# Kernel tuning notes

Measured on AMD Instinct MI355X. Metric: run time of the kernel, lower is better.

The kernel has to match this reference:

```python
import jax, jax.numpy as jnp
import numpy as np
import math

B, T, C = 2, 2048, 1024
N_HEAD = 16
HEAD_DIM = C // N_HEAD


def setup_inputs() -> dict:
    key = jax.random.key(0)
    k1, k2, k3 = jax.random.split(key, 3)
    x = jax.random.normal(k1, (B, T, C), dtype=jnp.float32)
    # causal mask: positions where mask == 0 get -inf
    mask = jnp.tril(jnp.ones((T, T), dtype=bool))[None, None, :, :]
    W_attn = jax.random.normal(k2, (C, 3 * C), dtype=jnp.float32) * (1.0 / math.sqrt(C))
    b_attn = jnp.zeros((3 * C,), dtype=jnp.float32)
    W_proj = jax.random.normal(k3, (C, C), dtype=jnp.float32) * (1.0 / math.sqrt(C))
    b_proj = jnp.zeros((C,), dtype=jnp.float32)
    return {"x": x, "mask": mask, "W_attn": W_attn, "b_attn": b_attn,
            "W_proj": W_proj, "b_proj": b_proj}


def reference(x, mask, W_attn, b_attn, W_proj, b_proj):
    Bx, Tx, Cx = x.shape
    qkv = x @ W_attn + b_attn                      # [B,T,3C]
    q, k, v = jnp.split(qkv, 3, axis=2)
    # [B,T,C] -> [B,H,T,D]
    q = q.reshape(Bx, Tx, N_HEAD, HEAD_DIM).transpose(0, 2, 1, 3)
    k = k.reshape(Bx, Tx, N_HEAD, HEAD_DIM).transpose(0, 2, 1, 3)
    v = v.reshape(Bx, Tx, N_HEAD, HEAD_DIM).transpose(0, 2, 1, 3)
    scale = 1.0 / math.sqrt(HEAD_DIM)
    att = jnp.einsum('bhqd,bhkd->bhqk', q, k) * scale   # [B,H,T,T]
    att = jnp.where(mask, att, -jnp.inf)
    att = jax.nn.softmax(att, axis=-1)
    y = jnp.einsum('bhqk,bhkd->bhqd', att, v)            # [B,H,T,D]
    y = y.transpose(0, 2, 1, 3).reshape(Bx, Tx, Cx)      # [B,T,C]
    return y @ W_proj + b_proj
```

## Files before the change

### kernel.cpp

```cpp
#include <hip/hip_runtime.h>
#include <hip/hip_bf16.h>
#include <cstdint>

typedef unsigned short u16;
typedef unsigned int u32;
typedef unsigned long long u64;
using f32x4 = __attribute__((ext_vector_type(4))) float;
using s16x8 = __attribute__((ext_vector_type(8))) short;
using u32x4 = __attribute__((ext_vector_type(4))) u32;

#define NB 2
#define NT 2048
#define NC 1024
#define NH 16
#define HD 64

__device__ __forceinline__ u16 f2b(float f) {
    unsigned u = __float_as_uint(f);
    unsigned r = (u + 0x7FFFu + ((u >> 16) & 1u)) >> 16;
    return (u16)r;
}

__device__ __forceinline__ u32 cvtpk(float a, float b) {
    u32 r;
    asm("v_cvt_pk_bf16_f32 %0, %1, %2" : "=v"(r) : "v"(a), "v"(b));
    return r;
}
__device__ __forceinline__ void swap32(u32& a, u32& b) {
    asm("v_permlane32_swap_b32 %0, %1" : "+v"(a), "+v"(b));
}
__device__ __forceinline__ void swap16(u32& a, u32& b) {
    asm("v_permlane16_swap_b32 %0, %1" : "+v"(a), "+v"(b));
}

__device__ __forceinline__ void gl_lds16(const void* g, const void* l) {
    __builtin_amdgcn_global_load_lds(
        (const __attribute__((address_space(1))) unsigned int*)g,
        (__attribute__((address_space(3))) unsigned int*)l, 16, 0, 0);
}

__global__ __launch_bounds__(256) void conv_bf16(const float* __restrict__ in,
                                                 u16* __restrict__ out, int n4) {
    int i = blockIdx.x * 256 + threadIdx.x;
    if (i >= n4) return;
    float4 v = ((const float4*)in)[i];
    u64 pack = (u64)f2b(v.x) | ((u64)f2b(v.y) << 16) |
               ((u64)f2b(v.z) << 32) | ((u64)f2b(v.w) << 48);
    ((u64*)out)[i] = pack;
}

__global__ __launch_bounds__(256) void transpose_bf16(const float* __restrict__ W,
                                                      u16* __restrict__ Wt,
                                                      int K, int N) {
    __shared__ u16 s[64][65];
    const int n0 = blockIdx.x * 64, k0 = blockIdx.y * 64;
    const int t = threadIdx.x;
    const int tr = t >> 4, tc4 = (t & 15) * 4;
#pragma unroll
    for (int i = 0; i < 4; i++) {
        int r = tr + i * 16;
        float4 v = *(const float4*)&W[(size_t)(k0 + r) * N + n0 + tc4];
        s[r][tc4 + 0] = f2b(v.x);
        s[r][tc4 + 1] = f2b(v.y);
        s[r][tc4 + 2] = f2b(v.z);
        s[r][tc4 + 3] = f2b(v.w);
    }
    __syncthreads();
#pragma unroll
    for (int i = 0; i < 4; i++) {
        int nl = tr + i * 16;
        u64 pack = (u64)s[tc4 + 0][nl] | ((u64)s[tc4 + 1][nl] << 16) |
                   ((u64)s[tc4 + 2][nl] << 32) | ((u64)s[tc4 + 3][nl] << 48);
        *(u64*)&Wt[(size_t)(n0 + nl) * K + k0 + tc4] = pack;
    }
}

template <int OUT_BF16>
__global__ __launch_bounds__(256) void gemm_bt(const u16* __restrict__ A,
                                               const u16* __restrict__ Bt,
                                               const float* __restrict__ bias,
                                               void* __restrict__ Cout,
                                               int M, int N, int K) {
    __shared__ u16 As[128 * 32];
    __shared__ u16 Bs[128 * 32];
    const int tid = threadIdx.x;
    const int lane = tid & 63, w = tid >> 6;
    const int m0 = blockIdx.y * 128, n0 = blockIdx.x * 128;
    const int wm = w >> 1, wn = w & 1;
    f32x4 acc[4][4] = {};

    const int srow = 32 * w + (lane >> 2);
    const int scol = (lane & 3) * 8;

    for (int k0 = 0; k0 < K; k0 += 32) {
        gl_lds16(&A[(size_t)(m0 + srow) * K + k0 + scol], &As[w * 1024 + lane * 8]);
        gl_lds16(&A[(size_t)(m0 + srow + 16) * K + k0 + scol], &As[w * 1024 + 512 + lane * 8]);
        gl_lds16(&Bt[(size_t)(n0 + srow) * K + k0 + scol], &Bs[w * 1024 + lane * 8]);
        gl_lds16(&Bt[(size_t)(n0 + srow + 16) * K + k0 + scol], &Bs[w * 1024 + 512 + lane * 8]);
        __syncthreads();

        s16x8 af[4], bf[4];
#pragma unroll
        for (int mt = 0; mt < 4; mt++)
            af[mt] = *(const s16x8*)&As[(wm * 64 + mt * 16 + (lane & 15)) * 32 + (lane >> 4) * 8];
#pragma unroll
        for (int nt = 0; nt < 4; nt++)
            bf[nt] = *(const s16x8*)&Bs[(wn * 64 + nt * 16 + (lane & 15)) * 32 + (lane >> 4) * 8];
#pragma unroll
        for (int mt = 0; mt < 4; mt++)
#pragma unroll
            for (int nt = 0; nt < 4; nt++)
                acc[mt][nt] = __builtin_amdgcn_mfma_f32_16x16x32_bf16(af[mt], bf[nt], acc[mt][nt], 0, 0, 0);
        __syncthreads();
    }

#pragma unroll
    for (int mt = 0; mt < 4; mt++) {
        int row = m0 + wm * 64 + mt * 16 + (lane >> 4) * 4;
#pragma unroll
        for (int nt = 0; nt < 4; nt++) {
            int col = n0 + wn * 64 + nt * 16 + (lane & 15);
            float bs = bias[col];
#pragma unroll
            for (int r = 0; r < 4; r++) {
                float v = acc[mt][nt][r] + bs;
                if (OUT_BF16)
                    ((u16*)Cout)[(size_t)(row + r) * N + col] = f2b(v);
                else
                    ((float*)Cout)[(size_t)(row + r) * N + col] = v;
            }
        }
    }
}

__global__ __launch_bounds__(256) void gemm_bt_n64(const u16* __restrict__ A,
                                                   const u16* __restrict__ Bt,
                                                   const float* __restrict__ bias,
                                                   float* __restrict__ Cout,
                                                   int M, int N, int K) {
    __shared__ u16 As[128 * 32];
    __shared__ u16 Bs[64 * 32];
    const int tid = threadIdx.x;
    const int lane = tid & 63, w = tid >> 6;
    const int m0 = blockIdx.y * 128, n0 = blockIdx.x * 64;
    f32x4 acc[2][4] = {};

    const int srow = 32 * w + (lane >> 2);
    const int srowB = 16 * w + (lane >> 2);
    const int scol = (lane & 3) * 8;

    for (int k0 = 0; k0 < K; k0 += 32) {
        gl_lds16(&A[(size_t)(m0 + srow) * K + k0 + scol], &As[w * 1024 + lane * 8]);
        gl_lds16(&A[(size_t)(m0 + srow + 16) * K + k0 + scol], &As[w * 1024 + 512 + lane * 8]);
        gl_lds16(&Bt[(size_t)(n0 + srowB) * K + k0 + scol], &Bs[w * 512 + lane * 8]);
        __syncthreads();

        s16x8 af[2], bf[4];
#pragma unroll
        for (int mt = 0; mt < 2; mt++)
            af[mt] = *(const s16x8*)&As[(w * 32 + mt * 16 + (lane & 15)) * 32 + (lane >> 4) * 8];
#pragma unroll
        for (int nt = 0; nt < 4; nt++)
            bf[nt] = *(const s16x8*)&Bs[(nt * 16 + (lane & 15)) * 32 + (lane >> 4) * 8];
#pragma unroll
        for (int mt = 0; mt < 2; mt++)
#pragma unroll
            for (int nt = 0; nt < 4; nt++)
                acc[mt][nt] = __builtin_amdgcn_mfma_f32_16x16x32_bf16(af[mt], bf[nt], acc[mt][nt], 0, 0, 0);
        __syncthreads();
    }

#pragma unroll
    for (int mt = 0; mt < 2; mt++) {
        int row = m0 + w * 32 + mt * 16 + (lane >> 4) * 4;
#pragma unroll
        for (int nt = 0; nt < 4; nt++) {
            int col = n0 + nt * 16 + (lane & 15);
            float bs = bias[col];
#pragma unroll
            for (int r = 0; r < 4; r++)
                Cout[(size_t)(row + r) * N + col] = acc[mt][nt][r] + bs;
        }
    }
}

__global__ __launch_bounds__(256) void v_transpose(const u16* __restrict__ qkv,
                                                   u16* __restrict__ Vt) {
    __shared__ __align__(16) u16 s[64][72];
    const int t0 = blockIdx.x * 64;
    const int b = blockIdx.y >> 4, h = blockIdx.y & 15;
    const int t = threadIdx.x;
    const int r = t >> 2, c0 = (t & 3) * 16;
    const u16* src = qkv + (size_t)b * NT * (3 * NC) + (size_t)(t0 + r) * (3 * NC) + 2 * NC + h * HD + c0;
    *(s16x8*)&s[r][c0] = *(const s16x8*)src;
    *(s16x8*)&s[r][c0 + 8] = *(const s16x8*)(src + 8);
    __syncthreads();
    u32 arr[8];
#pragma unroll
    for (int jj = 0; jj < 8; jj++)
        arr[jj] = (u32)s[c0 + 2 * jj][r] | ((u32)s[c0 + 2 * jj + 1][r] << 16);
    u16* dst = Vt + ((size_t)(b * NH + h) * HD + r) * NT + t0 + c0;
    u32x4 lo, hi;
    lo[0] = arr[0]; lo[1] = arr[1]; lo[2] = arr[2]; lo[3] = arr[3];
    hi[0] = arr[4]; hi[1] = arr[5]; hi[2] = arr[6]; hi[3] = arr[7];
    *(u32x4*)dst = lo;
    *(u32x4*)(dst + 8) = hi;
}

__global__ __launch_bounds__(256) void attn_kernel(const u16* __restrict__ qkv,
                                                   const u16* __restrict__ Vt,
                                                   u16* __restrict__ yb) {
    __shared__ u16 Kb[2][64 * 64];
    __shared__ u16 Vb[2][64 * 64];

    const int l = threadIdx.x & 63;
    const int q16 = l & 15, g = l >> 4;
    const int w = threadIdx.x >> 6;
    const int i0 = blockIdx.x;
    const int xcd = i0 & 7, idx = i0 >> 3;
    const int hh = xcd * 4 + (idx >> 4);
    const int pr = idx & 15;
    const int b = hh >> 4, h = hh & 15;

    const u16* qkvb = qkv + (size_t)b * NT * (3 * NC);

    const int srow = l >> 3;
    const int sc8 = (l & 7) ^ (srow & 7);
    const u16* kSrc0 = qkvb + NC + h * HD + (size_t)(8 * w + srow) * (3 * NC) + sc8 * 8;
    const u16* kSrc1 = kSrc0 + (size_t)32 * (3 * NC);
    const u16* vSrc0 = Vt + ((size_t)(b * NH + h) * HD + 8 * w + srow) * NT + sc8 * 8;
    const u16* vSrc1 = vSrc0 + (size_t)32 * NT;

    const float sc2 = 0.125f * 1.44269504088896340736f;
    const float SHIFT = 5.0f * 1.44269504088896340736f;
    const int sw = q16 & 7;

    auto STAGE = [&](int t) {
        const int buf = t & 1;
        const size_t kOff = (size_t)t * 64 * (3 * NC);
        const int vOff = t * 64;
        gl_lds16(kSrc0 + kOff, &Kb[buf][w * 512 + l * 8]);
        gl_lds16(kSrc1 + kOff, &Kb[buf][2048 + w * 512 + l * 8]);
        gl_lds16(vSrc0 + vOff, &Vb[buf][w * 512 + l * 8]);
        gl_lds16(vSrc1 + vOff, &Vb[buf][2048 + w * 512 + l * 8]);
    };

#pragma unroll 1
    for (int sc = 0; sc < 2; ++sc) {
        const int cc = (sc == 0) ? (31 - pr) : pr;
        const int qw = cc * 64 + 16 * w;
        const int nt = cc + 1;

        s16x8 qf[2];
#pragma unroll
        for (int kc = 0; kc < 2; kc++)
            qf[kc] = *(const s16x8*)(qkvb + (size_t)(qw + q16) * (3 * NC) + h * HD + kc * 32 + g * 8);

        f32x4 yacc[4] = {};
        float lsum = 0.f;

        STAGE(0);
        for (int t = 0; t < nt; ++t) {
            if (t + 1 < nt) {
                STAGE(t + 1);
                asm volatile("s_waitcnt vmcnt(4)" ::: "memory");
            } else {
                asm volatile("s_waitcnt vmcnt(0)" ::: "memory");
            }
            __builtin_amdgcn_s_barrier();

            const u16* Kc = Kb[t & 1];
            const u16* Vc = Vb[t & 1];

            s16x8 kf[4][2];
#pragma unroll
            for (int ii = 0; ii < 4; ii++)
#pragma unroll
                for (int kc = 0; kc < 2; kc++)
                    kf[ii][kc] = *(const s16x8*)&Kc[(16 * ii + q16) * 64 + ((4 * kc + g) ^ sw) * 8];

            s16x8 vf0[4];
#pragma unroll
            for (int dt = 0; dt < 4; dt++)
                vf0[dt] = *(const s16x8*)&Vc[(16 * dt + q16) * 64 + (g ^ sw) * 8];

            f32x4 sacc[4] = {};
            __builtin_amdgcn_s_setprio(1);
#pragma unroll
            for (int ii = 0; ii < 4; ii++)
#pragma unroll
                for (int kc = 0; kc < 2; kc++)
                    sacc[ii] = __builtin_amdgcn_mfma_f32_16x16x32_bf16(kf[ii][kc], qf[kc], sacc[ii], 0, 0, 0);
            __builtin_amdgcn_s_setprio(0);

            if (t == nt - 1) {
                const int kv0 = t * 64;
#pragma unroll
                for (int ii = 0; ii < 4; ii++)
#pragma unroll
                    for (int r = 0; r < 4; r++)
                        if (kv0 + 16 * ii + 4 * g + r > qw + q16) sacc[ii][r] = -1e30f;
            }

            float p[4][4];
            float ps = 0.f;
#pragma unroll
            for (int ii = 0; ii < 4; ii++)
#pragma unroll
                for (int r = 0; r < 4; r++) {
                    p[ii][r] = exp2f(fmaf(sacc[ii][r], sc2, -SHIFT));
                    ps += p[ii][r];
                }
            lsum += ps;

            s16x8 pfrag[2];
#pragma unroll
            for (int ks = 0; ks < 2; ks++) {
                u32 C0 = cvtpk(p[2 * ks][0], p[2 * ks][1]);
                u32 C1 = cvtpk(p[2 * ks][2], p[2 * ks][3]);
                u32 D0 = cvtpk(p[2 * ks + 1][0], p[2 * ks + 1][1]);
                u32 D1 = cvtpk(p[2 * ks + 1][2], p[2 * ks + 1][3]);
                swap32(C0, D0); swap16(C0, D0);
                swap32(C1, D1); swap16(C1, D1);
                u32x4 fr;
                fr[0] = C0; fr[1] = C1; fr[2] = D0; fr[3] = D1;
                pfrag[ks] = __builtin_bit_cast(s16x8, fr);
            }

            s16x8 vf1[4];
#pragma unroll
            for (int dt = 0; dt < 4; dt++)
                vf1[dt] = *(const s16x8*)&Vc[(16 * dt + q16) * 64 + ((4 + g) ^ sw) * 8];

            __builtin_amdgcn_s_setprio(1);
#pragma unroll
            for (int dt = 0; dt < 4; dt++)
                yacc[dt] = __builtin_amdgcn_mfma_f32_16x16x32_bf16(vf0[dt], pfrag[0], yacc[dt], 0, 0, 0);
#pragma unroll
            for (int dt = 0; dt < 4; dt++)
                yacc[dt] = __builtin_amdgcn_mfma_f32_16x16x32_bf16(vf1[dt], pfrag[1], yacc[dt], 0, 0, 0);
            __builtin_amdgcn_s_setprio(0);

            __builtin_amdgcn_s_barrier();
        }

        {
            lsum += __shfl_xor(lsum, 16);
            lsum += __shfl_xor(lsum, 32);
            float inv = 1.f / lsum;
            size_t rowoff = ((size_t)(b * NT + qw + q16)) * NC + h * HD;
#pragma unroll
            for (int dt = 0; dt < 4; dt++) {
                u32 lo = cvtpk(yacc[dt][0] * inv, yacc[dt][1] * inv);
                u32 hi = cvtpk(yacc[dt][2] * inv, yacc[dt][3] * inv);
                u64 pk = (u64)lo | ((u64)hi << 32);
                *(u64*)(yb + rowoff + 16 * dt + 4 * g) = pk;
            }
        }
    }
}

extern "C" void kernel_launch(void* const* d_in, const int* in_sizes, int n_in,
                              void* d_out, int out_size, void* d_ws, size_t ws_size,
                              hipStream_t stream) {
    const float* x  = (const float*)d_in[0];
    const float* Wa = (const float*)d_in[2];
    const float* ba = (const float*)d_in[3];
    const float* Wp = (const float*)d_in[4];
    const float* bp = (const float*)d_in[5];
    float* out = (float*)d_out;

    char* ws = (char*)d_ws;
    u16* xb  = (u16*)(ws);
    u16* WaT = (u16*)(ws + (8ull << 20));
    u16* WpT = (u16*)(ws + (14ull << 20));
    u16* qkv = (u16*)(ws + (16ull << 20));
    u16* yb  = (u16*)(ws + (40ull << 20));
    u16* Vtb = (u16*)(ws + (48ull << 20));

    const int M = NB * NT;

    conv_bf16<<<(M * NC / 4 + 255) / 256, 256, 0, stream>>>(x, xb, M * NC / 4);
    transpose_bf16<<<dim3(3 * NC / 64, NC / 64), 256, 0, stream>>>(Wa, WaT, NC, 3 * NC);
    transpose_bf16<<<dim3(NC / 64, NC / 64), 256, 0, stream>>>(Wp, WpT, NC, NC);

    gemm_bt<1><<<dim3(3 * NC / 128, M / 128), 256, 0, stream>>>(xb, WaT, ba, qkv, M, 3 * NC, NC);

    v_transpose<<<dim3(NT / 64, NB * NH), 256, 0, stream>>>(qkv, Vtb);

    attn_kernel<<<dim3(NB * NH * 16), 256, 0, stream>>>(qkv, Vtb, yb);

    gemm_bt_n64<<<dim3(NC / 64, M / 128), 256, 0, stream>>>(yb, WpT, bp, out, M, NC, NC);
}
```

Baseline: 128.7 us.

## Split attention KV loop across two wave groups per block with LDS merge

Doubles the attention block to 512 threads. Two groups of four waves each process half of the key/value tiles for the same query rows, using separate double-buffered K/V LDS regions. The partial outputs and row sums are then merged through shared memory. The aim is to shorten the serial KV loop per block and raise wave occupancy, at the cost of double the LDS, an extra merge step, and idle iterations when the tile count is odd. Normalisation uses a fixed shift with no running max, so the two halves combine by plain addition.

```diff
diff --git a/kernel.cpp b/kernel.cpp
--- a/kernel.cpp
+++ b/kernel.cpp
@@ -207,15 +207,16 @@
     *(u32x4*)(dst + 8) = hi;
 }
 
-__global__ __launch_bounds__(256) void attn_kernel(const u16* __restrict__ qkv,
+__global__ __launch_bounds__(512) void attn_kernel(const u16* __restrict__ qkv,
                                                    const u16* __restrict__ Vt,
                                                    u16* __restrict__ yb) {
-    __shared__ u16 Kb[2][64 * 64];
-    __shared__ u16 Vb[2][64 * 64];
+    __shared__ __align__(16) u16 Kb[2][2][64 * 64];
+    __shared__ __align__(16) u16 Vb[2][2][64 * 64];
 
     const int l = threadIdx.x & 63;
     const int q16 = l & 15, g = l >> 4;
-    const int w = threadIdx.x >> 6;
+    const int wv = threadIdx.x >> 6;
+    const int rg = wv & 3, hf = wv >> 2;
     const int i0 = blockIdx.x;
     const int xcd = i0 & 7, idx = i0 >> 3;
     const int hh = xcd * 4 + (idx >> 4);
@@ -226,9 +227,9 @@
 
     const int srow = l >> 3;
     const int sc8 = (l & 7) ^ (srow & 7);
-    const u16* kSrc0 = qkvb + NC + h * HD + (size_t)(8 * w + srow) * (3 * NC) + sc8 * 8;
+    const u16* kSrc0 = qkvb + NC + h * HD + (size_t)(8 * rg + srow) * (3 * NC) + sc8 * 8;
     const u16* kSrc1 = kSrc0 + (size_t)32 * (3 * NC);
-    const u16* vSrc0 = Vt + ((size_t)(b * NH + h) * HD + 8 * w + srow) * NT + sc8 * 8;
+    const u16* vSrc0 = Vt + ((size_t)(b * NH + h) * HD + 8 * rg + srow) * NT + sc8 * 8;
     const u16* vSrc1 = vSrc0 + (size_t)32 * NT;
 
     const float sc2 = 0.125f * 1.44269504088896340736f;
@@ -239,17 +240,20 @@
         const int buf = t & 1;
         const size_t kOff = (size_t)t * 64 * (3 * NC);
         const int vOff = t * 64;
-        gl_lds16(kSrc0 + kOff, &Kb[buf][w * 512 + l * 8]);
-        gl_lds16(kSrc1 + kOff, &Kb[buf][2048 + w * 512 + l * 8]);
-        gl_lds16(vSrc0 + vOff, &Vb[buf][w * 512 + l * 8]);
-        gl_lds16(vSrc1 + vOff, &Vb[buf][2048 + w * 512 + l * 8]);
+        gl_lds16(kSrc0 + kOff, &Kb[hf][buf][rg * 512 + l * 8]);
+        gl_lds16(kSrc1 + kOff, &Kb[hf][buf][2048 + rg * 512 + l * 8]);
+        gl_lds16(vSrc0 + vOff, &Vb[hf][buf][rg * 512 + l * 8]);
+        gl_lds16(vSrc1 + vOff, &Vb[hf][buf][2048 + rg * 512 + l * 8]);
     };
 
 #pragma unroll 1
     for (int sc = 0; sc < 2; ++sc) {
         const int cc = (sc == 0) ? (31 - pr) : pr;
-        const int qw = cc * 64 + 16 * w;
         const int nt = cc + 1;
+        const int h0 = (nt + 1) >> 1;
+        const int base = hf ? h0 : 0;
+        const int myN = hf ? (nt - h0) : h0;
+        const int qw = cc * 64 + 16 * rg;
 
         s16x8 qf[2];
 #pragma unroll
@@ -259,9 +263,11 @@
         f32x4 yacc[4] = {};
         float lsum = 0.f;
 
-        STAGE(0);
-        for (int t = 0; t < nt; ++t) {
-            if (t + 1 < nt) {
+        if (myN > 0) STAGE(base);
+        for (int u = 0; u < h0; ++u) {
+            const int t = base + u;
+            const bool act = (u < myN);
+            if (act && (u + 1 < myN)) {
                 STAGE(t + 1);
                 asm volatile("s_waitcnt vmcnt(4)" ::: "memory");
             } else {
@@ -269,82 +275,101 @@
             }
             __builtin_amdgcn_s_barrier();
 
-            const u16* Kc = Kb[t & 1];
-            const u16* Vc = Vb[t & 1];
-
-            s16x8 kf[4][2];
-#pragma unroll
-            for (int ii = 0; ii < 4; ii++)
-#pragma unroll
-                for (int kc = 0; kc < 2; kc++)
-                    kf[ii][kc] = *(const s16x8*)&Kc[(16 * ii + q16) * 64 + ((4 * kc + g) ^ sw) * 8];
-
-            s16x8 vf0[4];
-#pragma unroll
-            for (int dt = 0; dt < 4; dt++)
-                vf0[dt] = *(const s16x8*)&Vc[(16 * dt + q16) * 64 + (g ^ sw) * 8];
-
-            f32x4 sacc[4] = {};
-            __builtin_amdgcn_s_setprio(1);
-#pragma unroll
-            for (int ii = 0; ii < 4; ii++)
-#pragma unroll
-                for (int kc = 0; kc < 2; kc++)
-                    sacc[ii] = __builtin_amdgcn_mfma_f32_16x16x32_bf16(kf[ii][kc], qf[kc], sacc[ii], 0, 0, 0);
-            __builtin_amdgcn_s_setprio(0);
-
-            if (t == nt - 1) {
-                const int kv0 = t * 64;
+            if (act) {
+                const u16* Kc = &Kb[hf][t & 1][0];
+                const u16* Vc = &Vb[hf][t & 1][0];
+
+                s16x8 kf[4][2];
 #pragma unroll
                 for (int ii = 0; ii < 4; ii++)
 #pragma unroll
-                    for (int r = 0; r < 4; r++)
-                        if (kv0 + 16 * ii + 4 * g + r > qw + q16) sacc[ii][r] = -1e30f;
+                    for (int kc = 0; kc < 2; kc++)
+                        kf[ii][kc] = *(const s16x8*)&Kc[(16 * ii + q16) * 64 + ((4 * kc + g) ^ sw) * 8];
+
+                s16x8 vf0[4];
+#pragma unroll
+                for (int dt = 0; dt < 4; dt++)
+                    vf0[dt] = *(const s16x8*)&Vc[(16 * dt + q16) * 64 + (g ^ sw) * 8];
+
+                f32x4 sacc[4] = {};
+                __builtin_amdgcn_s_setprio(1);
+#pragma unroll
+                for (int ii = 0; ii < 4; ii++)
+#pragma unroll
+                    for (int kc = 0; kc < 2; kc++)
+                        sacc[ii] = __builtin_amdgcn_mfma_f32_16x16x32_bf16(kf[ii][kc], qf[kc], sacc[ii], 0, 0, 0);
+                __builtin_amdgcn_s_setprio(0);
+
+                if (t == cc) {
+                    const int kv0 = t * 64;
+#pragma unroll
+                    for (int ii = 0; ii < 4; ii++)
+#pragma unroll
+                        for (int r = 0; r < 4; r++)
+                            if (kv0 + 16 * ii + 4 * g + r > qw + q16) sacc[ii][r] = -1e30f;
+                }
+
+                float p[4][4];
+                float ps = 0.f;
+#pragma unroll
+                for (int ii = 0; ii < 4; ii++)
+#pragma unroll
+                    for (int r = 0; r < 4; r++) {
+                        p[ii][r] = exp2f(fmaf(sacc[ii][r], sc2, -SHIFT));
+                        ps += p[ii][r];
+                    }
+                lsum += ps;
+
+                s16x8 pfrag[2];
+#pragma unroll
+                for (int ks = 0; ks < 2; ks++) {
+                    u32 C0 = cvtpk(p[2 * ks][0], p[2 * ks][1]);
+                    u32 C1 = cvtpk(p[2 * ks][2], p[2 * ks][3]);
+                    u32 D0 = cvtpk(p[2 * ks + 1][0], p[2 * ks + 1][1]);
+                    u32 D1 = cvtpk(p[2 * ks + 1][2], p[2 * ks + 1][3]);
+                    swap32(C0, D0); swap16(C0, D0);
+                    swap32(C1, D1); swap16(C1, D1);
+                    u32x4 fr;
+                    fr[0] = C0; fr[1] = C1; fr[2] = D0; fr[3] = D1;
+                    pfrag[ks] = __builtin_bit_cast(s16x8, fr);
+                }
+
+                s16x8 vf1[4];
+#pragma unroll
+                for (int dt = 0; dt < 4; dt++)
+                    vf1[dt] = *(const s16x8*)&Vc[(16 * dt + q16) * 64 + ((4 + g) ^ sw) * 8];
+
+                __builtin_amdgcn_s_setprio(1);
+#pragma unroll
+                for (int dt = 0; dt < 4; dt++)
+                    yacc[dt] = __builtin_amdgcn_mfma_f32_16x16x32_bf16(vf0[dt], pfrag[0], yacc[dt], 0, 0, 0);
+#pragma unroll
+                for (int dt = 0; dt < 4; dt++)
+                    yacc[dt] = __builtin_amdgcn_mfma_f32_16x16x32_bf16(vf1[dt], pfrag[1], yacc[dt], 0, 0, 0);
+                __builtin_amdgcn_s_setprio(0);
             }
-
-            float p[4][4];
-            float ps = 0.f;
-#pragma unroll
-            for (int ii = 0; ii < 4; ii++)
-#pragma unroll
-                for (int r = 0; r < 4; r++) {
-                    p[ii][r] = exp2f(fmaf(sacc[ii][r], sc2, -SHIFT));
-                    ps += p[ii][r];
-                }
-            lsum += ps;
-
-            s16x8 pfrag[2];
-#pragma unroll
-            for (int ks = 0; ks < 2; ks++) {
-                u32 C0 = cvtpk(p[2 * ks][0], p[2 * ks][1]);
-                u32 C1 = cvtpk(p[2 * ks][2], p[2 * ks][3]);
-                u32 D0 = cvtpk(p[2 * ks + 1][0], p[2 * ks + 1][1]);
-                u32 D1 = cvtpk(p[2 * ks + 1][2], p[2 * ks + 1][3]);
-                swap32(C0, D0); swap16(C0, D0);
-                swap32(C1, D1); swap16(C1, D1);
-                u32x4 fr;
-                fr[0] = C0; fr[1] = C1; fr[2] = D0; fr[3] = D1;
-                pfrag[ks] = __builtin_bit_cast(s16x8, fr);
-            }
-
-            s16x8 vf1[4];
-#pragma unroll
-            for (int dt = 0; dt < 4; dt++)
-                vf1[dt] = *(const s16x8*)&Vc[(16 * dt + q16) * 64 + ((4 + g) ^ sw) * 8];
-
-            __builtin_amdgcn_s_setprio(1);
-#pragma unroll
-            for (int dt = 0; dt < 4; dt++)
-                yacc[dt] = __builtin_amdgcn_mfma_f32_16x16x32_bf16(vf0[dt], pfrag[0], yacc[dt], 0, 0, 0);
-#pragma unroll
-            for (int dt = 0; dt < 4; dt++)
-                yacc[dt] = __builtin_amdgcn_mfma_f32_16x16x32_bf16(vf1[dt], pfrag[1], yacc[dt], 0, 0, 0);
-            __builtin_amdgcn_s_setprio(0);
 
             __builtin_amdgcn_s_barrier();
         }
 
-        {
+        float* mY = (float*)&Kb[1][0][0];
+        float* mL = (float*)&Vb[1][0][0];
+        if (hf == 1) {
+#pragma unroll
+            for (int dt = 0; dt < 4; dt++)
+#pragma unroll
+                for (int r = 0; r < 4; r++)
+                    mY[(rg * 16 + dt * 4 + r) * 64 + l] = yacc[dt][r];
+            mL[rg * 64 + l] = lsum;
+        }
+        __syncthreads();
+        if (hf == 0) {
+#pragma unroll
+            for (int dt = 0; dt < 4; dt++)
+#pragma unroll
+                for (int r = 0; r < 4; r++)
+                    yacc[dt][r] += mY[(rg * 16 + dt * 4 + r) * 64 + l];
+            lsum += mL[rg * 64 + l];
             lsum += __shfl_xor(lsum, 16);
             lsum += __shfl_xor(lsum, 32);
             float inv = 1.f / lsum;
@@ -357,6 +382,7 @@
                 *(u64*)(yb + rowoff + 16 * dt + 4 * g) = pk;
             }
         }
+        __syncthreads();
     }
 }
 
@@ -388,7 +414,7 @@
 
     v_transpose<<<dim3(NT / 64, NB * NH), 256, 0, stream>>>(qkv, Vtb);
 
-    attn_kernel<<<dim3(NB * NH * 16), 256, 0, stream>>>(qkv, Vtb, yb);
+    attn_kernel<<<dim3(NB * NH * 16), 512, 0, stream>>>(qkv, Vtb, yb);
 
     gemm_bt_n64<<<dim3(NC / 64, M / 128), 256, 0, stream>>>(yb, WpT, bp, out, M, NC, NC);
 }
```

Result: faster. 122.2 us (-5.0%).
